# Performance work log

Measured on AMD Instinct MI355X. Metric: run time of the kernel, lower is better.

Reference implementation:

```python
import jax, jax.numpy as jnp
import numpy as np

DIM = 64
HEADS = 16
HEAD_DIM = DIM // HEADS  # 4
CHUNK = 128
LN_EPS = 1e-5


def _ln(v, w, b):
    mu = jnp.mean(v, axis=-1, keepdims=True)
    var = jnp.var(v, axis=-1, keepdims=True)
    return (v - mu) * jax.lax.rsqrt(var + LN_EPS) * w + b


def setup_inputs() -> dict:
    key = jax.random.key(0)
    ks = jax.random.split(key, 16)
    B, C, H, W = 8, 64, 128, 128
    s = 0.02
    inp = {
        "x": jax.random.normal(ks[0], (B, C, H, W), jnp.float32),
        "text_embed": jax.random.normal(ks[1], (B, C, H, W), jnp.float32),
        # Linear weights stored as [in, out] (torch uses [out, in]; math identical via x @ W)
        "q_w": jax.random.normal(ks[2], (DIM, DIM), jnp.float32) * s,
        "q_b": jnp.zeros((DIM,), jnp.float32),
        "k_w": jax.random.normal(ks[3], (DIM, DIM), jnp.float32) * s,
        "k_b": jnp.zeros((DIM,), jnp.float32),
        "v_w": jax.random.normal(ks[4], (DIM, DIM), jnp.float32) * s,
        "v_b": jnp.zeros((DIM,), jnp.float32),
        "o_w": jax.random.normal(ks[5], (DIM, DIM), jnp.float32) * s,
        "o_b": jnp.zeros((DIM,), jnp.float32),
        "ln1_w": jnp.ones((DIM,), jnp.float32),
        "ln1_b": jnp.zeros((DIM,), jnp.float32),
        "ln2_w": jnp.ones((DIM,), jnp.float32),
        "ln2_b": jnp.zeros((DIM,), jnp.float32),
        "fc1_w": jax.random.normal(ks[6], (DIM, 4 * DIM), jnp.float32) * s,
        "fc1_b": jnp.zeros((4 * DIM,), jnp.float32),
        "fc2_w": jax.random.normal(ks[7], (4 * DIM, DIM), jnp.float32) * s,
        "fc2_b": jnp.zeros((DIM,), jnp.float32),
        # 1x1 conv as [out_ch, in_ch]
        "conv_w": jax.random.normal(ks[8], (DIM, DIM), jnp.float32) * s,
        "conv_b": jnp.zeros((DIM,), jnp.float32),
        # FiLM MLP: pooled_channels=64*4*4=1024 -> 128 -> 128
        "m1_w": jax.random.normal(ks[9], (1024, 2 * DIM), jnp.float32) * s,
        "m1_b": jnp.zeros((2 * DIM,), jnp.float32),
        "m2_w": jax.random.normal(ks[10], (2 * DIM, 2 * DIM), jnp.float32) * s,
        "m2_b": jnp.zeros((2 * DIM,), jnp.float32),
    }
    return inp


def reference(x, text_embed, q_w, q_b, k_w, k_b, v_w, v_b, o_w, o_b,
              ln1_w, ln1_b, ln2_w, ln2_b, fc1_w, fc1_b, fc2_w, fc2_b,
              conv_w, conv_b, m1_w, m1_b, m2_w, m2_b):
    B, C, H, W = x.shape
    N = H * W
    Nc = N // CHUNK  # number of local chunks (block-diagonal attention)
    scale = jnp.sqrt(jnp.float32(HEAD_DIM))

    prior_flat = text_embed.reshape(B, C, N).transpose(0, 2, 1)  # [B,N,C]
    x_flat = x.reshape(B, C, N).transpose(0, 2, 1)               # [B,N,C]

    prior_norm = _ln(prior_flat, ln1_w, ln1_b)
    Q = prior_norm @ q_w + q_b
    K = x_flat @ k_w + k_b
    V = x_flat @ v_w + v_b

    # blocked heads: [B, Nc, CHUNK, HEADS, HEAD_DIM]
    Qb = Q.reshape(B, Nc, CHUNK, HEADS, HEAD_DIM)
    Kb = K.reshape(B, Nc, CHUNK, HEADS, HEAD_DIM)
    Vb = V.reshape(B, Nc, CHUNK, HEADS, HEAD_DIM)

    scores = jnp.einsum('bnqhd,bnkhd->bnhqk', Qb, Kb) / scale  # [B,Nc,H,CHUNK,CHUNK]
    probs = jax.nn.softmax(scores, axis=-1)
    attn = jnp.einsum('bnhqk,bnkhd->bnqhd', probs, Vb).reshape(B, N, DIM)

    attn = attn @ o_w + o_b
    h = attn + prior_flat
    h_norm = _ln(h, ln2_w, ln2_b)
    ffn = jax.nn.gelu(h_norm @ fc1_w + fc1_b, approximate=False) @ fc2_w + fc2_b
    h = ffn + h

    h4 = h.transpose(0, 2, 1).reshape(B, DIM, H, W)
    conv = jnp.einsum('bihw,oi->bohw', h4, conv_w) + conv_b[None, :, None, None]
    out = conv + x  # TIAM output

    # FiLM: adaptive_avg_pool2d to (4,4) (H,W divisible by 4)
    te = text_embed.reshape(B, C, 4, H // 4, 4, W // 4).mean(axis=(3, 5))  # [B,C,4,4]
    te = te.reshape(B, -1)  # [B, 1024]
    hmlp = jax.nn.leaky_relu(te @ m1_w + m1_b, negative_slope=0.01)
    gb = hmlp @ m2_w + m2_b  # [B, 128]
    gamma = gb[:, :DIM][:, :, None, None]
    beta = gb[:, DIM:][:, :, None, None]
    return (1.0 + gamma) * out + beta
```

## Files before the change

kernel.cpp:

```cpp
#include <hip/hip_runtime.h>
#include <hip/hip_bf16.h>

#define NB 8
#define NTOK 16384
#define TOTTOK (NB*NTOK)

typedef __hip_bfloat16 bf16;
typedef __attribute__((ext_vector_type(8))) short bfrag;
typedef __attribute__((ext_vector_type(4))) float ffrag;

#define MFMA(a,b,c) __builtin_amdgcn_mfma_f32_16x16x32_bf16(a,b,c,0,0,0)

__device__ __forceinline__ float b2f(bf16 v){ return __bfloat162float(v); }
__device__ __forceinline__ bf16 f2b(float v){ return __float2bfloat16(v); }
__device__ __forceinline__ float bfu(unsigned short u){
    union { float f; unsigned v; } x; x.v = ((unsigned)u) << 16; return x.f; }
__device__ __forceinline__ unsigned short ubits(float f){
    union { bf16 b; unsigned short u; } x; x.b = __float2bfloat16(f); return x.u; }
__device__ __forceinline__ unsigned short bu(bf16 b){
    union { bf16 b; unsigned short u; } x; x.b = b; return x.u; }
__device__ __forceinline__ void ld4(const bf16* p, float* f){
    uint2 r = *(const uint2*)p;
    f[0]=bfu(r.x & 0xffff); f[1]=bfu(r.x >> 16); f[2]=bfu(r.y & 0xffff); f[3]=bfu(r.y >> 16);
}
__device__ __forceinline__ bfrag ld_frag(const bf16* p, int stride){
    int lane = threadIdx.x & 63;
    return *(const bfrag*)(p + (lane & 15)*stride + (lane >> 4)*8);
}

#define WI_QKV   0
#define WI_OW    13824
#define WI_CW    18432
#define WI_W1    23040
#define WI_W2    41472
#define WI_CONST 57856
#define WI_TOT   58752

__global__ __launch_bounds__(256) void wprep_kernel(
    const float* __restrict__ qw, const float* __restrict__ kw, const float* __restrict__ vw,
    const float* __restrict__ ow, const float* __restrict__ cw,
    const float* __restrict__ w1, const float* __restrict__ w2,
    const float* __restrict__ ln1w, const float* __restrict__ ln1b,
    const float* __restrict__ qb, const float* __restrict__ kb_, const float* __restrict__ vb,
    const float* __restrict__ ob, const float* __restrict__ ln2w, const float* __restrict__ ln2b,
    const float* __restrict__ b1, const float* __restrict__ b2, const float* __restrict__ cb,
    bf16* __restrict__ WI)
{
    int gid = blockIdx.x*256 + threadIdx.x;
    if (gid >= WI_TOT) return;
    float v = 0.f;
    if (gid < WI_OW){
        int m = gid / 4608, r = gid % 4608;
        int o = r / 72, ii = r % 72;
        const float* src = (m==0)? qw : (m==1)? kw : vw;
        if (ii < 64) v = src[ii*64 + o];
    } else if (gid < WI_CW){
        int r = gid - WI_OW;
        int o = r / 72, ii = r % 72;
        if (ii < 64) v = ow[ii*64 + o];
    } else if (gid < WI_W1){
        int r = gid - WI_CW;
        int co = r / 72, ii = r % 72;
        if (ii < 64) v = cw[co*64 + ii];
    } else if (gid < WI_W2){
        int r = gid - WI_W1;
        int gg = r / 2304, rr = r % 2304;
        int ol = rr / 72, ii = rr % 72;
        if (ii < 64) v = w1[ii*256 + gg*32 + ol];
    } else if (gid < WI_CONST){
        int a = gid - WI_W2;
        int o = a >> 8, ra = a & 255;
        int blk = ra >> 3, wi = ra & 7;
        int k = ((blk ^ (o & 7)) << 3) | wi;
        v = w2[k*64 + o];
    } else {
        int r = gid - WI_CONST;
        if      (r <  64) v = ln1w[r];
        else if (r < 128) v = ln1b[r-64];
        else if (r < 192) v = qb[r-128];
        else if (r < 256) v = kb_[r-192];
        else if (r < 320) v = vb[r-256];
        else if (r < 384) v = ob[r-320];
        else if (r < 448) v = ln2w[r-384];
        else if (r < 512) v = ln2b[r-448];
        else if (r < 768) v = b1[r-512];
        else if (r < 832) v = b2[r-768];
        else              v = cb[r-832];
    }
    WI[gid] = f2b(v);
}

__global__ __launch_bounds__(256) void transpose_kernel(
    const float* __restrict__ x, const float* __restrict__ te,
    bf16* __restrict__ xT, bf16* __restrict__ teT, float* __restrict__ pool)
{
    __shared__ bf16 T[64*66];
    int blk = blockIdx.x;
    int tile = blk & 255, b = blk >> 8;
    int t0 = tile * 64;
    const size_t sbase = (size_t)b*64*NTOK + t0;
    const size_t obase = ((size_t)b*NTOK + t0)*64;
    int tid = threadIdx.x;
    #pragma unroll
    for (int p = 0; p < 4; ++p){
        int c = p*16 + (tid >> 4), j4 = (tid & 15)*4;
        float4 v = *(const float4*)(x + sbase + (size_t)c*NTOK + j4);
        bf16* tp = T + c*66 + j4;
        tp[0]=f2b(v.x); tp[1]=f2b(v.y); tp[2]=f2b(v.z); tp[3]=f2b(v.w);
    }
    __syncthreads();
    #pragma unroll
    for (int p = 0; p < 4; ++p){
        int j = p*16 + (tid >> 4), c4 = (tid & 15)*4;
        uint2 o;
        o.x = (unsigned)bu(T[(c4+0)*66 + j]) | ((unsigned)bu(T[(c4+1)*66 + j]) << 16);
        o.y = (unsigned)bu(T[(c4+2)*66 + j]) | ((unsigned)bu(T[(c4+3)*66 + j]) << 16);
        *(uint2*)(xT + obase + (size_t)j*64 + c4) = o;
    }
    __syncthreads();
    #pragma unroll
    for (int p = 0; p < 4; ++p){
        int c = p*16 + (tid >> 4), j4 = (tid & 15)*4;
        float4 v = *(const float4*)(te + sbase + (size_t)c*NTOK + j4);
        bf16* tp = T + c*66 + j4;
        tp[0]=f2b(v.x); tp[1]=f2b(v.y); tp[2]=f2b(v.z); tp[3]=f2b(v.w);
    }
    __syncthreads();
    #pragma unroll
    for (int p = 0; p < 4; ++p){
        int j = p*16 + (tid >> 4), c4 = (tid & 15)*4;
        uint2 o;
        o.x = (unsigned)bu(T[(c4+0)*66 + j]) | ((unsigned)bu(T[(c4+1)*66 + j]) << 16);
        o.y = (unsigned)bu(T[(c4+2)*66 + j]) | ((unsigned)bu(T[(c4+3)*66 + j]) << 16);
        *(uint2*)(teT + obase + (size_t)j*64 + c4) = o;
    }
    if (tid < 128){
        int c = tid >> 1, hf = tid & 1;
        float s = 0.f;
        #pragma unroll
        for (int u = 0; u < 32; ++u) s += b2f(T[c*66 + hf*32 + u]);
        int h = t0 >> 7;
        int w0 = t0 & 127;
        int region = (h >> 5)*4 + ((w0 + hf*32) >> 5);
        atomicAdd(pool + b*1024 + c*16 + region, s);
    }
}

__global__ __launch_bounds__(128) void film_kernel(const float* __restrict__ pool,
        const float* __restrict__ m1w, const float* __restrict__ m1b,
        const float* __restrict__ m2w, const float* __restrict__ m2b,
        float* __restrict__ gb){
    int b = blockIdx.x; int j = threadIdx.x;
    __shared__ float tel[1024];
    __shared__ float hm[128];
    for (int i = j; i < 1024; i += 128) tel[i] = pool[b*1024 + i] * (1.f/1024.f);
    __syncthreads();
    float s = m1b[j];
    for (int i = 0; i < 1024; ++i) s = fmaf(tel[i], m1w[i*128 + j], s);
    hm[j] = (s > 0.f) ? s : 0.01f*s;
    __syncthreads();
    float g = m2b[j];
    for (int i = 0; i < 128; ++i) g = fmaf(hm[i], m2w[i*128 + j], g);
    gb[b*128 + j] = g;
}

#define OFF_TE2 0
#define OFF_XT  16384
#define OFF_PN  34816
#define OFF_WT  53248
#define OFF_W2T 47616
#define OFF_CON 80896
#define SCALE_Q 0.72134752044448170f

__device__ __forceinline__ void ln_phase(const bf16* S, bf16* D,
                                         const bf16* Wt, const bf16* Bs, int tid)
{
    int tok = tid >> 1, hf = tid & 1;
    float vals[32];
    float s = 0.f, s2 = 0.f;
    #pragma unroll
    for (int u8 = 0; u8 < 4; ++u8){
        int k = (u8 + tok) & 3;
        uint4 v = *(const uint4*)(S + tok*64 + hf*32 + k*8);
        const unsigned* ap = &v.x;
        float* vp = vals + u8*8;
        #pragma unroll
        for (int e = 0; e < 4; ++e){
            float lo = bfu(ap[e] & 0xffff), hi = bfu(ap[e] >> 16);
            vp[e*2] = lo; vp[e*2+1] = hi;
            s += lo + hi;
            s2 = fmaf(lo, lo, fmaf(hi, hi, s2));
        }
    }
    s  += __shfl_xor(s, 1, 64);
    s2 += __shfl_xor(s2, 1, 64);
    float mean = s * (1.f/64.f);
    float var  = s2 * (1.f/64.f) - mean*mean;
    float rstd = rsqrtf(var + 1e-5f);
    #pragma unroll
    for (int u8 = 0; u8 < 4; ++u8){
        int k = (u8 + tok) & 3;
        int cc0 = hf*32 + k*8;
        uint4 wv = *(const uint4*)(Wt + cc0);
        uint4 bv = *(const uint4*)(Bs + cc0);
        const unsigned* wp = &wv.x;
        const unsigned* bp = &bv.x;
        uint4 o; unsigned* op = &o.x;
        #pragma unroll
        for (int e = 0; e < 4; ++e){
            float lo = (vals[u8*8+e*2]  -mean)*rstd*bfu(wp[e] & 0xffff) + bfu(bp[e] & 0xffff);
            float hi = (vals[u8*8+e*2+1]-mean)*rstd*bfu(wp[e] >> 16)    + bfu(bp[e] >> 16);
            op[e] = (unsigned)ubits(lo) | ((unsigned)ubits(hi) << 16);
        }
        *(uint4*)(D + tok*72 + cc0) = o;
    }
}

__global__ __launch_bounds__(256,2) void mega_kernel(
    const bf16* __restrict__ xT, const bf16* __restrict__ teT, const float* __restrict__ x,
    const bf16* __restrict__ WI, const float* __restrict__ gb, float* __restrict__ out)
{
    __shared__ __align__(16) char sm[81920];
    bf16* TE2 = (bf16*)(sm + OFF_TE2);
    bf16* XT  = (bf16*)(sm + OFF_XT);
    bf16* PN  = (bf16*)(sm + OFF_PN);
    bf16* WT  = (bf16*)(sm + OFF_WT);
    bf16* VT  = (bf16*)(sm + OFF_WT);
    bf16* OWT = (bf16*)(sm + OFF_WT);
    bf16* W1S = (bf16*)(sm + OFF_PN);
    bf16* P   = (bf16*)(sm + OFF_PN + 4608);
    bf16* CWs = (bf16*)(sm + OFF_PN);
    bf16* W2T = (bf16*)(sm + OFF_W2T);
    bf16* CON = (bf16*)(sm + OFF_CON);
    bf16* OT  = (bf16*)(sm + OFF_TE2);

    int tid = threadIdx.x;
    int w = tid >> 6, lane = tid & 63;
    int g = lane >> 4, c = lane & 15;
    int t0g = blockIdx.x * 128;
    int b = t0g >> 14, n0 = t0g & (NTOK-1);
    const ffrag fz = {0.f,0.f,0.f,0.f};

    {
        const uint4* gx = (const uint4*)(xT + (size_t)t0g*64);
        const uint4* gt = (const uint4*)(teT + (size_t)t0g*64);
        #pragma unroll
        for (int p = 0; p < 4; ++p){
            int i = tid + p*256;
            int tok = i >> 3, seg = i & 7;
            *(uint4*)(XT + tok*72 + seg*8) = gx[i];
            ((uint4*)TE2)[i] = gt[i];
        }
        const uint4* wq = (const uint4*)(WI + WI_QKV);
        for (int i = tid; i < 1728; i += 256) ((uint4*)WT)[i] = wq[i];
        if (tid < 16) ((uint4*)CON)[tid] = ((const uint4*)(WI + WI_CONST))[tid];
    }
    __syncthreads();
    ln_phase(TE2, PN, CON, CON + 64, tid);
    __syncthreads();
    {
        if (tid < 24) ((uint4*)CON)[tid] = ((const uint4*)(WI + WI_CONST + 128))[tid];
        ffrag accQ[2][4], accK[2][4], accV[2][4];
        #pragma unroll
        for (int mi=0;mi<2;++mi) for (int nt=0;nt<4;++nt){ accQ[mi][nt]=fz; accK[mi][nt]=fz; accV[mi][nt]=fz; }
        bfrag aQ[2][2], aX[2][2];
        #pragma unroll
        for (int mi=0;mi<2;++mi) for (int k2=0;k2<2;++k2){
            aQ[mi][k2] = ld_frag(PN + (w*32 + mi*16)*72 + k2*32, 72);
            aX[mi][k2] = ld_frag(XT + (w*32 + mi*16)*72 + k2*32, 72);
        }
        for (int nt = 0; nt < 4; ++nt){
            #pragma unroll
            for (int k2 = 0; k2 < 2; ++k2){
                bfrag bq2 = ld_frag(WT +        nt*16*72 + k2*32, 72);
                bfrag bk2 = ld_frag(WT + 4608 + nt*16*72 + k2*32, 72);
                bfrag bv2 = ld_frag(WT + 9216 + nt*16*72 + k2*32, 72);
                #pragma unroll
                for (int mi=0;mi<2;++mi){
                    accQ[mi][nt] = MFMA(aQ[mi][k2], bq2, accQ[mi][nt]);
                    accK[mi][nt] = MFMA(aX[mi][k2], bk2, accK[mi][nt]);
                    accV[mi][nt] = MFMA(aX[mi][k2], bv2, accV[mi][nt]);
                }
            }
        }
        __syncthreads();
        int rq = g*4;
        #pragma unroll
        for (int mi=0;mi<2;++mi) for (int nt=0;nt<4;++nt){
            int n = nt*16 + c;
            float bq3 = b2f(CON[n]), bk3 = b2f(CON[64+n]), bv3 = b2f(CON[128+n]);
            #pragma unroll
            for (int r=0;r<4;++r){
                int m = w*32 + mi*16 + rq + r;
                PN[m*72 + n] = f2b((accQ[mi][nt][r] + bq3) * SCALE_Q);
                XT[m*72 + n] = f2b(accK[mi][nt][r] + bk3);
                int kp = (m & 15)*8 + (m >> 4);
                VT[(5*(n>>2) + (n&3))*136 + kp] = f2b(accV[mi][nt][r] + bv3);
            }
        }
        {
            int row = 5*(tid >> 4) + 4, col8 = (tid & 15)*8;
            uint4 ov; ov.x = ov.y = ov.z = ov.w = 0x3f803f80u;
            *(uint4*)(VT + row*136 + col8) = ov;
        }
    }
    __syncthreads();
    {
        int kb = w >> 1;
        bfrag bq[8];
        #pragma unroll
        for (int nt = 0; nt < 8; ++nt) bq[nt] = ld_frag(XT + nt*16*72 + kb*32, 72);
        __syncthreads();
        bf16* Pw = XT + w*2048;
        #pragma unroll 1
        for (int hh = 0; hh < 4; ++hh){
            int h = w*4 + hh;
            int ag = (h & 7) >> 1;
            bfrag bv4[4];
            #pragma unroll
            for (int ks = 0; ks < 4; ++ks) bv4[ks] = ld_frag(VT + (5*h)*136 + ks*32, 136);
            #pragma unroll 2
            for (int qt = 0; qt < 8; ++qt){
                int q = qt*16 + c;
                uint2 qv = *(const uint2*)(PN + q*72 + h*4);
                union { bfrag f; uint2 u[2]; } A;
                uint2 z2; z2.x = 0u; z2.y = 0u;
                uint2 sel = (g == ag) ? qv : z2;
                if (hh & 1){ A.u[0] = z2;  A.u[1] = sel; }
                else       { A.u[0] = sel; A.u[1] = z2;  }
                ffrag acc[8];
                #pragma unroll
                for (int nt = 0; nt < 8; ++nt) acc[nt] = MFMA(A.f, bq[nt], fz);
                #pragma unroll
                for (int nt = 0; nt < 8; ++nt){
                    #pragma unroll
                    for (int r = 0; r < 4; ++r) acc[nt][r] = exp2f(acc[nt][r]);
                }
                #pragma unroll
                for (int r = 0; r < 4; ++r){
                    uint4 pk;
                    pk.x = (unsigned)ubits(acc[0][r]) | ((unsigned)ubits(acc[1][r]) << 16);
                    pk.y = (unsigned)ubits(acc[2][r]) | ((unsigned)ubits(acc[3][r]) << 16);
                    pk.z = (unsigned)ubits(acc[4][r]) | ((unsigned)ubits(acc[5][r]) << 16);
                    pk.w = (unsigned)ubits(acc[6][r]) | ((unsigned)ubits(acc[7][r]) << 16);
                    int row = 4*g + r;
                    *(uint4*)(Pw + row*128 + (((c ^ row) & 15) << 3)) = pk;
                }
                ffrag og = fz;
                #pragma unroll
                for (int ks = 0; ks < 4; ++ks){
                    bfrag ap = *(const bfrag*)(Pw + c*128 + ((((ks*4 + g) ^ c) & 15) << 3));
                    og = MFMA(ap, bv4[ks], og);
                }
                #pragma unroll
                for (int r = 0; r < 4; ++r){
                    float lr = __shfl(og[r], (lane & 48) | 4, 64);
                    if (c < 4)
                        PN[(qt*16 + 4*g + r)*72 + h*4 + c] = f2b(og[r] / lr);
                }
            }
        }
    }
    __syncthreads();
    {
        const uint4* oi = (const uint4*)(WI + WI_OW);
        for (int i = tid; i < 576; i += 256) ((uint4*)OWT)[i] = oi[i];
        if (tid < 24) ((uint4*)CON)[tid] = ((const uint4*)(WI + WI_CONST + 320))[tid];
        __syncthreads();
        ffrag acc2[2][4];
        #pragma unroll
        for (int mi=0;mi<2;++mi) for (int nt=0;nt<4;++nt) acc2[mi][nt] = fz;
        bfrag af2[2][2];
        #pragma unroll
        for (int mi=0;mi<2;++mi) for (int k2=0;k2<2;++k2)
            af2[mi][k2] = ld_frag(PN + (w*32 + mi*16)*72 + k2*32, 72);
        #pragma unroll
        for (int nt=0;nt<4;++nt){
            #pragma unroll
            for (int k2=0;k2<2;++k2){
                bfrag bf_ = ld_frag(OWT + nt*16*72 + k2*32, 72);
                #pragma unroll
                for (int mi=0;mi<2;++mi) acc2[mi][nt] = MFMA(af2[mi][k2], bf_, acc2[mi][nt]);
            }
        }
        __syncthreads();
        int rq = g*4;
        #pragma unroll
        for (int mi=0;mi<2;++mi) for (int nt=0;nt<4;++nt){
            int n = nt*16 + c;
            float bo = b2f(CON[n]);
            #pragma unroll
            for (int r=0;r<4;++r){
                int m = w*32 + mi*16 + rq + r;
                XT[m*72 + n] = f2b(acc2[mi][nt][r] + bo);
            }
        }
    }
    __syncthreads();
    for (int j = tid; j < 1024; j += 256){
        int tok = j >> 3, c8 = (j & 7)*8;
        uint4 a = *(const uint4*)(TE2 + tok*64 + c8);
        uint4 bq = *(const uint4*)(XT + tok*72 + c8);
        const unsigned* ap = &a.x; const unsigned* bp = &bq.x;
        uint4 o; unsigned* op = &o.x;
        #pragma unroll
        for (int e = 0; e < 4; ++e){
            float lo = bfu(ap[e] & 0xffff) + bfu(bp[e] & 0xffff);
            float hi = bfu(ap[e] >> 16)    + bfu(bp[e] >> 16);
            op[e] = (unsigned)ubits(lo) | ((unsigned)ubits(hi) << 16);
        }
        *(uint4*)(TE2 + tok*64 + c8) = o;
    }
    __syncthreads();
    ln_phase(TE2, XT, CON + 64, CON + 128, tid);
    __syncthreads();
    {
        const uint4* w2i = (const uint4*)(WI + WI_W2);
        for (int i = tid; i < 2048; i += 256) ((uint4*)W2T)[i] = w2i[i];
        if (tid < 48) ((uint4*)CON)[tid] = ((const uint4*)(WI + WI_CONST + 512))[tid];
        bfrag af[2][2];
        #pragma unroll
        for (int mi=0;mi<2;++mi) for (int k2=0;k2<2;++k2)
            af[mi][k2] = ld_frag(XT + (w*32 + mi*16)*72 + k2*32, 72);
        ffrag acc2[2][4];
        #pragma unroll
        for (int mi=0;mi<2;++mi) for (int nt=0;nt<4;++nt) acc2[mi][nt] = fz;
        int rq = g*4;
        const uint4* w1i = (const uint4*)(WI + WI_W1);
        uint4 pA = w1i[tid];
        uint4 pB = pA;
        if (tid < 32) pB = w1i[256 + tid];
        for (int gg = 0; gg < 8; ++gg){
            __syncthreads();
            ((uint4*)W1S)[tid] = pA;
            if (tid < 32) ((uint4*)W1S)[256 + tid] = pB;
            if (gg < 7){
                pA = w1i[(gg+1)*288 + tid];
                if (tid < 32) pB = w1i[(gg+1)*288 + 256 + tid];
            }
            __syncthreads();
            ffrag accg[2][2];
            #pragma unroll
            for (int mi=0;mi<2;++mi) for (int ntl=0;ntl<2;++ntl) accg[mi][ntl] = fz;
            #pragma unroll
            for (int ntl=0;ntl<2;++ntl){
                #pragma unroll
                for (int k2=0;k2<2;++k2){
                    bfrag bf_ = ld_frag(W1S + ntl*16*72 + k2*32, 72);
                    #pragma unroll
                    for (int mi=0;mi<2;++mi) accg[mi][ntl] = MFMA(af[mi][k2], bf_, accg[mi][ntl]);
                }
            }
            #pragma unroll
            for (int mi=0;mi<2;++mi) for (int ntl=0;ntl<2;++ntl){
                int n = ntl*16 + c;
                float bb = b2f(CON[gg*32 + n]);
                #pragma unroll
                for (int r=0;r<4;++r){
                    int m = w*32 + mi*16 + rq + r;
                    float xv = accg[mi][ntl][r] + bb;
                    P[m*32 + ((((n>>3) ^ ((m>>1)&3)) << 3) | (n & 7))] =
                        f2b(0.5f*xv*(1.f + erff(xv*0.70710678118654752f)));
                }
            }
            #pragma unroll
            for (int mi=0;mi<2;++mi){
                int rr = w*32 + mi*16 + c;
                bfrag ap = *(const bfrag*)(P + rr*32 + ((g ^ ((rr>>1)&3)) << 3));
                #pragma unroll
                for (int nt=0;nt<4;++nt){
                    int n = nt*16 + c;
                    int chunk = gg*4 + g;
                    bfrag bf2 = *(const bfrag*)(W2T + n*256 + ((chunk ^ (n&7)) << 3));
                    acc2[mi][nt] = MFMA(ap, bf2, acc2[mi][nt]);
                }
            }
        }
        #pragma unroll
        for (int mi=0;mi<2;++mi) for (int nt=0;nt<4;++nt){
            int n = nt*16 + c;
            float bb = b2f(CON[256+n]);
            #pragma unroll
            for (int r=0;r<4;++r){
                int m = w*32 + mi*16 + rq + r;
                XT[m*72 + n] = f2b(acc2[mi][nt][r] + bb + b2f(TE2[m*64 + n]));
            }
        }
    }
    __syncthreads();
    {
        const uint4* ci = (const uint4*)(WI + WI_CW);
        for (int i = tid; i < 576; i += 256) ((uint4*)CWs)[i] = ci[i];
        __syncthreads();
        bfrag ac[2];
        #pragma unroll
        for (int k2=0;k2<2;++k2) ac[k2] = ld_frag(CWs + (w*16)*72 + k2*32, 72);
        int rq = g*4;
        for (int nt = 0; nt < 8; ++nt){
            ffrag accc = fz;
            #pragma unroll
            for (int k2=0;k2<2;++k2){
                bfrag bh = ld_frag(XT + nt*16*72 + k2*32, 72);
                accc = MFMA(ac[k2], bh, accc);
            }
            int tok = nt*16 + c;
            #pragma unroll
            for (int r=0;r<4;++r){
                int co = w*16 + rq + r;
                OT[co*128 + tok] = f2b(accc[r] + b2f(CON[320+co]));
            }
        }
    }
    __syncthreads();
    {
        int cc = tid >> 2, seg = (tid & 3)*32;
        float gamma = 1.f + gb[b*128 + cc];
        float beta  = gb[b*128 + 64 + cc];
        const size_t gbase = (size_t)b*64*NTOK + (size_t)cc*NTOK + n0 + seg;
        #pragma unroll
        for (int u = 0; u < 8; ++u){
            float cv[4];
            ld4(OT + cc*128 + seg + u*4, cv);
            float4 xv = *(const float4*)(x + gbase + u*4);
            float4 ov;
            ov.x = fmaf(gamma, cv[0]+xv.x, beta);
            ov.y = fmaf(gamma, cv[1]+xv.y, beta);
            ov.z = fmaf(gamma, cv[2]+xv.z, beta);
            ov.w = fmaf(gamma, cv[3]+xv.w, beta);
            *(float4*)(out + gbase + u*4) = ov;
        }
    }
}

extern "C" void kernel_launch(void* const* d_in, const int* in_sizes, int n_in,
                              void* d_out, int out_size, void* d_ws, size_t ws_size,
                              hipStream_t stream){
    const float* x   = (const float*)d_in[0];
    const float* te  = (const float*)d_in[1];
    const float* qw  = (const float*)d_in[2];
    const float* qb  = (const float*)d_in[3];
    const float* kw  = (const float*)d_in[4];
    const float* kb  = (const float*)d_in[5];
    const float* vw  = (const float*)d_in[6];
    const float* vb  = (const float*)d_in[7];
    const float* ow  = (const float*)d_in[8];
    const float* ob  = (const float*)d_in[9];
    const float* ln1w= (const float*)d_in[10];
    const float* ln1b= (const float*)d_in[11];
    const float* ln2w= (const float*)d_in[12];
    const float* ln2b= (const float*)d_in[13];
    const float* w1  = (const float*)d_in[14];
    const float* b1  = (const float*)d_in[15];
    const float* w2  = (const float*)d_in[16];
    const float* b2  = (const float*)d_in[17];
    const float* cw  = (const float*)d_in[18];
    const float* cb  = (const float*)d_in[19];
    const float* m1w = (const float*)d_in[20];
    const float* m1b = (const float*)d_in[21];
    const float* m2w = (const float*)d_in[22];
    const float* m2b = (const float*)d_in[23];

    char* ws = (char*)d_ws;
    const size_t BUF = (size_t)TOTTOK*64*2;
    bf16* xT  = (bf16*)(ws);
    bf16* teT = (bf16*)(ws + BUF);
    float* pool = (float*)(ws + 2*BUF);
    float* gbp  = (float*)(ws + 2*BUF + 32768);
    bf16* WI    = (bf16*)(ws + 2*BUF + 36864);

    hipMemsetAsync(pool, 0, 8*1024*sizeof(float), stream);
    wprep_kernel<<<(WI_TOT + 255)/256, 256, 0, stream>>>(
        qw, kw, vw, ow, cw, w1, w2,
        ln1w, ln1b, qb, kb, vb, ob, ln2w, ln2b, b1, b2, cb, WI);
    transpose_kernel<<<2048, 256, 0, stream>>>(x, te, xT, teT, pool);
    film_kernel<<<8, 128, 0, stream>>>(pool, m1w, m1b, m2w, m2b, gbp);
    mega_kernel<<<TOTTOK/128, 256, 0, stream>>>(xT, teT, x, WI, gbp, (float*)d_out);
}
```

Measured before the change: 350.5 us.

## Double fused-kernel block to 512 threads and use fast GELU approximation

The fused per-chunk kernel now runs with 512 threads (8 waves) per 128-token block instead of 256. Each wave owns 16 rows instead of 32, and the attention, LN, conv and output phases are re-partitioned to match, including new V and P layouts. The exact erf GELU is replaced by a sigmoid-style exp2/rcp approximation, and the division in the softmax normalisation becomes a hardware reciprocal. This aims to raise wave-level parallelism and cut transcendental cost, at the price of more synchronisation per block, small accuracy loss, and register pressure from the tighter launch bounds.

After: 317.2 us. 1.11x faster.

```diff
diff --git a/kernel.cpp b/kernel.cpp
--- a/kernel.cpp
+++ b/kernel.cpp
@@ -22,6 +22,15 @@
 __device__ __forceinline__ void ld4(const bf16* p, float* f){
     uint2 r = *(const uint2*)p;
     f[0]=bfu(r.x & 0xffff); f[1]=bfu(r.x >> 16); f[2]=bfu(r.y & 0xffff); f[3]=bfu(r.y >> 16);
+}
+__device__ __forceinline__ float fastrcp(float x){
+    float r; asm("v_rcp_f32 %0, %1" : "=v"(r) : "v"(x)); return r; }
+__device__ __forceinline__ float gelu_t(float x){
+    float x2 = x*x;
+    float y  = x * fmaf(x2, 0.1029425f, 2.3022077f);
+    float z  = exp2f(y);
+    float rc = fastrcp(z + 1.f);
+    return x - x*rc;
 }
 __device__ __forceinline__ bfrag ld_frag(const bf16* p, int stride){
     int lane = threadIdx.x & 63;
@@ -175,13 +184,15 @@
 __device__ __forceinline__ void ln_phase(const bf16* S, bf16* D,
                                          const bf16* Wt, const bf16* Bs, int tid)
 {
-    int tok = tid >> 1, hf = tid & 1;
-    float vals[32];
+    int tok = tid >> 2, q4 = tid & 3;
+    float vals[16];
+    int op2[2];
     float s = 0.f, s2 = 0.f;
     #pragma unroll
-    for (int u8 = 0; u8 < 4; ++u8){
-        int k = (u8 + tok) & 3;
-        uint4 v = *(const uint4*)(S + tok*64 + hf*32 + k*8);
+    for (int u8 = 0; u8 < 2; ++u8){
+        int o = (q4*2 + u8) ^ (tok & 7);
+        op2[u8] = o;
+        uint4 v = *(const uint4*)(S + tok*64 + o*8);
         const unsigned* ap = &v.x;
         float* vp = vals + u8*8;
         #pragma unroll
@@ -192,31 +203,30 @@
             s2 = fmaf(lo, lo, fmaf(hi, hi, s2));
         }
     }
-    s  += __shfl_xor(s, 1, 64);
-    s2 += __shfl_xor(s2, 1, 64);
+    s  += __shfl_xor(s, 1, 64);  s2 += __shfl_xor(s2, 1, 64);
+    s  += __shfl_xor(s, 2, 64);  s2 += __shfl_xor(s2, 2, 64);
     float mean = s * (1.f/64.f);
     float var  = s2 * (1.f/64.f) - mean*mean;
     float rstd = rsqrtf(var + 1e-5f);
     #pragma unroll
-    for (int u8 = 0; u8 < 4; ++u8){
-        int k = (u8 + tok) & 3;
-        int cc0 = hf*32 + k*8;
+    for (int u8 = 0; u8 < 2; ++u8){
+        int cc0 = op2[u8]*8;
         uint4 wv = *(const uint4*)(Wt + cc0);
         uint4 bv = *(const uint4*)(Bs + cc0);
         const unsigned* wp = &wv.x;
         const unsigned* bp = &bv.x;
-        uint4 o; unsigned* op = &o.x;
+        uint4 o; unsigned* opp = &o.x;
         #pragma unroll
         for (int e = 0; e < 4; ++e){
             float lo = (vals[u8*8+e*2]  -mean)*rstd*bfu(wp[e] & 0xffff) + bfu(bp[e] & 0xffff);
             float hi = (vals[u8*8+e*2+1]-mean)*rstd*bfu(wp[e] >> 16)    + bfu(bp[e] >> 16);
-            op[e] = (unsigned)ubits(lo) | ((unsigned)ubits(hi) << 16);
+            opp[e] = (unsigned)ubits(lo) | ((unsigned)ubits(hi) << 16);
         }
         *(uint4*)(D + tok*72 + cc0) = o;
     }
 }
 
-__global__ __launch_bounds__(256,2) void mega_kernel(
+__global__ __launch_bounds__(512,4) void mega_kernel(
     const bf16* __restrict__ xT, const bf16* __restrict__ teT, const float* __restrict__ x,
     const bf16* __restrict__ WI, const float* __restrict__ gb, float* __restrict__ out)
 {
@@ -245,14 +255,14 @@
         const uint4* gx = (const uint4*)(xT + (size_t)t0g*64);
         const uint4* gt = (const uint4*)(teT + (size_t)t0g*64);
         #pragma unroll
-        for (int p = 0; p < 4; ++p){
-            int i = tid + p*256;
+        for (int p = 0; p < 2; ++p){
+            int i = tid + p*512;
             int tok = i >> 3, seg = i & 7;
             *(uint4*)(XT + tok*72 + seg*8) = gx[i];
             ((uint4*)TE2)[i] = gt[i];
         }
         const uint4* wq = (const uint4*)(WI + WI_QKV);
-        for (int i = tid; i < 1728; i += 256) ((uint4*)WT)[i] = wq[i];
+        for (int i = tid; i < 1728; i += 512) ((uint4*)WT)[i] = wq[i];
         if (tid < 16) ((uint4*)CON)[tid] = ((const uint4*)(WI + WI_CONST))[tid];
     }
     __syncthreads();
@@ -260,14 +270,14 @@
     __syncthreads();
     {
         if (tid < 24) ((uint4*)CON)[tid] = ((const uint4*)(WI + WI_CONST + 128))[tid];
-        ffrag accQ[2][4], accK[2][4], accV[2][4];
-        #pragma unroll
-        for (int mi=0;mi<2;++mi) for (int nt=0;nt<4;++nt){ accQ[mi][nt]=fz; accK[mi][nt]=fz; accV[mi][nt]=fz; }
-        bfrag aQ[2][2], aX[2][2];
-        #pragma unroll
-        for (int mi=0;mi<2;++mi) for (int k2=0;k2<2;++k2){
-            aQ[mi][k2] = ld_frag(PN + (w*32 + mi*16)*72 + k2*32, 72);
-            aX[mi][k2] = ld_frag(XT + (w*32 + mi*16)*72 + k2*32, 72);
+        ffrag accQ[4], accK[4], accV[4];
+        #pragma unroll
+        for (int nt=0;nt<4;++nt){ accQ[nt]=fz; accK[nt]=fz; accV[nt]=fz; }
+        bfrag aQ[2], aX[2];
+        #pragma unroll
+        for (int k2=0;k2<2;++k2){
+            aQ[k2] = ld_frag(PN + (w*16)*72 + k2*32, 72);
+            aX[k2] = ld_frag(XT + (w*16)*72 + k2*32, 72);
         }
         for (int nt = 0; nt < 4; ++nt){
             #pragma unroll
@@ -275,30 +285,27 @@
                 bfrag bq2 = ld_frag(WT +        nt*16*72 + k2*32, 72);
                 bfrag bk2 = ld_frag(WT + 4608 + nt*16*72 + k2*32, 72);
                 bfrag bv2 = ld_frag(WT + 9216 + nt*16*72 + k2*32, 72);
-                #pragma unroll
-                for (int mi=0;mi<2;++mi){
-                    accQ[mi][nt] = MFMA(aQ[mi][k2], bq2, accQ[mi][nt]);
-                    accK[mi][nt] = MFMA(aX[mi][k2], bk2, accK[mi][nt]);
-                    accV[mi][nt] = MFMA(aX[mi][k2], bv2, accV[mi][nt]);
-                }
+                accQ[nt] = MFMA(aQ[k2], bq2, accQ[nt]);
+                accK[nt] = MFMA(aX[k2], bk2, accK[nt]);
+                accV[nt] = MFMA(aX[k2], bv2, accV[nt]);
             }
         }
         __syncthreads();
         int rq = g*4;
         #pragma unroll
-        for (int mi=0;mi<2;++mi) for (int nt=0;nt<4;++nt){
+        for (int nt=0;nt<4;++nt){
             int n = nt*16 + c;
             float bq3 = b2f(CON[n]), bk3 = b2f(CON[64+n]), bv3 = b2f(CON[128+n]);
             #pragma unroll
             for (int r=0;r<4;++r){
-                int m = w*32 + mi*16 + rq + r;
-                PN[m*72 + n] = f2b((accQ[mi][nt][r] + bq3) * SCALE_Q);
-                XT[m*72 + n] = f2b(accK[mi][nt][r] + bk3);
-                int kp = (m & 15)*8 + (m >> 4);
-                VT[(5*(n>>2) + (n&3))*136 + kp] = f2b(accV[mi][nt][r] + bv3);
-            }
-        }
-        {
+                int m = w*16 + rq + r;
+                PN[m*72 + n] = f2b((accQ[nt][r] + bq3) * SCALE_Q);
+                XT[m*72 + n] = f2b(accK[nt][r] + bk3);
+                int kp = ((m >> 6) << 6) + (m & 15)*4 + ((m >> 4) & 3);
+                VT[(5*(n>>2) + (n&3))*136 + kp] = f2b(accV[nt][r] + bv3);
+            }
+        }
+        if (tid < 256){
             int row = 5*(tid >> 4) + 4, col8 = (tid & 15)*8;
             uint4 ov; ov.x = ov.y = ov.z = ov.w = 0x3f803f80u;
             *(uint4*)(VT + row*136 + col8) = ov;
@@ -306,19 +313,19 @@
     }
     __syncthreads();
     {
-        int kb = w >> 1;
         bfrag bq[8];
         #pragma unroll
-        for (int nt = 0; nt < 8; ++nt) bq[nt] = ld_frag(XT + nt*16*72 + kb*32, 72);
+        for (int nt = 0; nt < 8; ++nt) bq[nt] = ld_frag(XT + nt*16*72 + (w>>2)*32, 72);
         __syncthreads();
-        bf16* Pw = XT + w*2048;
+        bf16* Pw = XT + w*1024;
         #pragma unroll 1
-        for (int hh = 0; hh < 4; ++hh){
-            int h = w*4 + hh;
-            int ag = (h & 7) >> 1;
+        for (int hh = 0; hh < 2; ++hh){
+            int h = w*2 + hh;
+            int ag = w & 3;
             bfrag bv4[4];
             #pragma unroll
-            for (int ks = 0; ks < 4; ++ks) bv4[ks] = ld_frag(VT + (5*h)*136 + ks*32, 136);
+            for (int kk = 0; kk < 4; ++kk)
+                bv4[kk] = ld_frag(VT + (5*h)*136 + (kk>>1)*64 + (kk&1)*32, 136);
             #pragma unroll 2
             for (int qt = 0; qt < 8; ++qt){
                 int q = qt*16 + c;
@@ -326,37 +333,38 @@
                 union { bfrag f; uint2 u[2]; } A;
                 uint2 z2; z2.x = 0u; z2.y = 0u;
                 uint2 sel = (g == ag) ? qv : z2;
-                if (hh & 1){ A.u[0] = z2;  A.u[1] = sel; }
-                else       { A.u[0] = sel; A.u[1] = z2;  }
-                ffrag acc[8];
-                #pragma unroll
-                for (int nt = 0; nt < 8; ++nt) acc[nt] = MFMA(A.f, bq[nt], fz);
-                #pragma unroll
-                for (int nt = 0; nt < 8; ++nt){
-                    #pragma unroll
-                    for (int r = 0; r < 4; ++r) acc[nt][r] = exp2f(acc[nt][r]);
-                }
-                #pragma unroll
-                for (int r = 0; r < 4; ++r){
-                    uint4 pk;
-                    pk.x = (unsigned)ubits(acc[0][r]) | ((unsigned)ubits(acc[1][r]) << 16);
-                    pk.y = (unsigned)ubits(acc[2][r]) | ((unsigned)ubits(acc[3][r]) << 16);
-                    pk.z = (unsigned)ubits(acc[4][r]) | ((unsigned)ubits(acc[5][r]) << 16);
-                    pk.w = (unsigned)ubits(acc[6][r]) | ((unsigned)ubits(acc[7][r]) << 16);
-                    int row = 4*g + r;
-                    *(uint4*)(Pw + row*128 + (((c ^ row) & 15) << 3)) = pk;
-                }
+                if (hh){ A.u[0] = z2;  A.u[1] = sel; }
+                else   { A.u[0] = sel; A.u[1] = z2;  }
                 ffrag og = fz;
                 #pragma unroll
-                for (int ks = 0; ks < 4; ++ks){
-                    bfrag ap = *(const bfrag*)(Pw + c*128 + ((((ks*4 + g) ^ c) & 15) << 3));
-                    og = MFMA(ap, bv4[ks], og);
+                for (int kh = 0; kh < 2; ++kh){
+                    ffrag acc[4];
+                    #pragma unroll
+                    for (int nt = 0; nt < 4; ++nt) acc[nt] = MFMA(A.f, bq[kh*4+nt], fz);
+                    #pragma unroll
+                    for (int nt = 0; nt < 4; ++nt){
+                        #pragma unroll
+                        for (int r = 0; r < 4; ++r) acc[nt][r] = exp2f(acc[nt][r]);
+                    }
+                    #pragma unroll
+                    for (int r = 0; r < 4; ++r){
+                        uint2 pk;
+                        pk.x = (unsigned)ubits(acc[0][r]) | ((unsigned)ubits(acc[1][r]) << 16);
+                        pk.y = (unsigned)ubits(acc[2][r]) | ((unsigned)ubits(acc[3][r]) << 16);
+                        int row = 4*g + r;
+                        *(uint2*)(Pw + row*64 + (((c>>1) ^ (row&7)) << 3) + ((c&1) << 2)) = pk;
+                    }
+                    #pragma unroll
+                    for (int ks = 0; ks < 2; ++ks){
+                        bfrag ap = *(const bfrag*)(Pw + c*64 + (((ks*4 + g) ^ (c&7)) << 3));
+                        og = MFMA(ap, bv4[kh*2 + ks], og);
+                    }
                 }
                 #pragma unroll
                 for (int r = 0; r < 4; ++r){
                     float lr = __shfl(og[r], (lane & 48) | 4, 64);
                     if (c < 4)
-                        PN[(qt*16 + 4*g + r)*72 + h*4 + c] = f2b(og[r] / lr);
+                        PN[(qt*16 + 4*g + r)*72 + h*4 + c] = f2b(og[r] * fastrcp(lr));
                 }
             }
         }
@@ -364,50 +372,49 @@
     __syncthreads();
     {
         const uint4* oi = (const uint4*)(WI + WI_OW);
-        for (int i = tid; i < 576; i += 256) ((uint4*)OWT)[i] = oi[i];
+        for (int i = tid; i < 576; i += 512) ((uint4*)OWT)[i] = oi[i];
         if (tid < 24) ((uint4*)CON)[tid] = ((const uint4*)(WI + WI_CONST + 320))[tid];
         __syncthreads();
-        ffrag acc2[2][4];
-        #pragma unroll
-        for (int mi=0;mi<2;++mi) for (int nt=0;nt<4;++nt) acc2[mi][nt] = fz;
-        bfrag af2[2][2];
-        #pragma unroll
-        for (int mi=0;mi<2;++mi) for (int k2=0;k2<2;++k2)
-            af2[mi][k2] = ld_frag(PN + (w*32 + mi*16)*72 + k2*32, 72);
+        ffrag acc2[4];
+        #pragma unroll
+        for (int nt=0;nt<4;++nt) acc2[nt] = fz;
+        bfrag af2[2];
+        #pragma unroll
+        for (int k2=0;k2<2;++k2)
+            af2[k2] = ld_frag(PN + (w*16)*72 + k2*32, 72);
         #pragma unroll
         for (int nt=0;nt<4;++nt){
             #pragma unroll
             for (int k2=0;k2<2;++k2){
                 bfrag bf_ = ld_frag(OWT + nt*16*72 + k2*32, 72);
-                #pragma unroll
-                for (int mi=0;mi<2;++mi) acc2[mi][nt] = MFMA(af2[mi][k2], bf_, acc2[mi][nt]);
+                acc2[nt] = MFMA(af2[k2], bf_, acc2[nt]);
             }
         }
         __syncthreads();
         int rq = g*4;
         #pragma unroll
-        for (int mi=0;mi<2;++mi) for (int nt=0;nt<4;++nt){
+        for (int nt=0;nt<4;++nt){
             int n = nt*16 + c;
             float bo = b2f(CON[n]);
             #pragma unroll
             for (int r=0;r<4;++r){
-                int m = w*32 + mi*16 + rq + r;
-                XT[m*72 + n] = f2b(acc2[mi][nt][r] + bo);
-            }
-        }
-    }
-    __syncthreads();
-    for (int j = tid; j < 1024; j += 256){
+                int m = w*16 + rq + r;
+                XT[m*72 + n] = f2b(acc2[nt][r] + bo);
+            }
+        }
+    }
+    __syncthreads();
+    for (int j = tid; j < 1024; j += 512){
         int tok = j >> 3, c8 = (j & 7)*8;
         uint4 a = *(const uint4*)(TE2 + tok*64 + c8);
-        uint4 bq = *(const uint4*)(XT + tok*72 + c8);
-        const unsigned* ap = &a.x; const unsigned* bp = &bq.x;
-        uint4 o; unsigned* op = &o.x;
+        uint4 bq2 = *(const uint4*)(XT + tok*72 + c8);
+        const unsigned* ap = &a.x; const unsigned* bp = &bq2.x;
+        uint4 o; unsigned* opp = &o.x;
         #pragma unroll
         for (int e = 0; e < 4; ++e){
             float lo = bfu(ap[e] & 0xffff) + bfu(bp[e] & 0xffff);
             float hi = bfu(ap[e] >> 16)    + bfu(bp[e] >> 16);
-            op[e] = (unsigned)ubits(lo) | ((unsigned)ubits(hi) << 16);
+            opp[e] = (unsigned)ubits(lo) | ((unsigned)ubits(hi) << 16);
         }
         *(uint4*)(TE2 + tok*64 + c8) = o;
     }
@@ -416,87 +423,83 @@
     __syncthreads();
     {
         const uint4* w2i = (const uint4*)(WI + WI_W2);
-        for (int i = tid; i < 2048; i += 256) ((uint4*)W2T)[i] = w2i[i];
+        for (int i = tid; i < 2048; i += 512) ((uint4*)W2T)[i] = w2i[i];
         if (tid < 48) ((uint4*)CON)[tid] = ((const uint4*)(WI + WI_CONST + 512))[tid];
-        bfrag af[2][2];
-        #pragma unroll
-        for (int mi=0;mi<2;++mi) for (int k2=0;k2<2;++k2)
-            af[mi][k2] = ld_frag(XT + (w*32 + mi*16)*72 + k2*32, 72);
-        ffrag acc2[2][4];
-        #pragma unroll
-        for (int mi=0;mi<2;++mi) for (int nt=0;nt<4;++nt) acc2[mi][nt] = fz;
+        bfrag af[2];
+        #pragma unroll
+        for (int k2=0;k2<2;++k2)
+            af[k2] = ld_frag(XT + (w*16)*72 + k2*32, 72);
+        ffrag acc2[4];
+        #pragma unroll
+        for (int nt=0;nt<4;++nt) acc2[nt] = fz;
         int rq = g*4;
         const uint4* w1i = (const uint4*)(WI + WI_W1);
-        uint4 pA = w1i[tid];
-        uint4 pB = pA;
-        if (tid < 32) pB = w1i[256 + tid];
+        uint4 pA;
+        if (tid < 288) pA = w1i[tid];
         for (int gg = 0; gg < 8; ++gg){
             __syncthreads();
-            ((uint4*)W1S)[tid] = pA;
-            if (tid < 32) ((uint4*)W1S)[256 + tid] = pB;
-            if (gg < 7){
-                pA = w1i[(gg+1)*288 + tid];
-                if (tid < 32) pB = w1i[(gg+1)*288 + 256 + tid];
+            if (tid < 288){
+                ((uint4*)W1S)[tid] = pA;
+                if (gg < 7) pA = w1i[(gg+1)*288 + tid];
             }
             __syncthreads();
-            ffrag accg[2][2];
-            #pragma unroll
-            for (int mi=0;mi<2;++mi) for (int ntl=0;ntl<2;++ntl) accg[mi][ntl] = fz;
+            ffrag accg[2];
+            #pragma unroll
+            for (int ntl=0;ntl<2;++ntl) accg[ntl] = fz;
             #pragma unroll
             for (int ntl=0;ntl<2;++ntl){
                 #pragma unroll
                 for (int k2=0;k2<2;++k2){
                     bfrag bf_ = ld_frag(W1S + ntl*16*72 + k2*32, 72);
-                    #pragma unroll
-                    for (int mi=0;mi<2;++mi) accg[mi][ntl] = MFMA(af[mi][k2], bf_, accg[mi][ntl]);
+                    accg[ntl] = MFMA(af[k2], bf_, accg[ntl]);
                 }
             }
             #pragma unroll
-            for (int mi=0;mi<2;++mi) for (int ntl=0;ntl<2;++ntl){
+            for (int ntl=0;ntl<2;++ntl){
                 int n = ntl*16 + c;
                 float bb = b2f(CON[gg*32 + n]);
                 #pragma unroll
                 for (int r=0;r<4;++r){
-                    int m = w*32 + mi*16 + rq + r;
-                    float xv = accg[mi][ntl][r] + bb;
-                    P[m*32 + ((((n>>3) ^ ((m>>1)&3)) << 3) | (n & 7))] =
-                        f2b(0.5f*xv*(1.f + erff(xv*0.70710678118654752f)));
+                    int m = w*16 + rq + r;
+                    float xv = accg[ntl][r] + bb;
+                    P[m*32 + ((((n>>3) ^ ((m>>1)&3)) << 3) | (n & 7))] = f2b(gelu_t(xv));
                 }
             }
-            #pragma unroll
-            for (int mi=0;mi<2;++mi){
-                int rr = w*32 + mi*16 + c;
+            {
+                int rr = w*16 + c;
                 bfrag ap = *(const bfrag*)(P + rr*32 + ((g ^ ((rr>>1)&3)) << 3));
                 #pragma unroll
                 for (int nt=0;nt<4;++nt){
                     int n = nt*16 + c;
                     int chunk = gg*4 + g;
                     bfrag bf2 = *(const bfrag*)(W2T + n*256 + ((chunk ^ (n&7)) << 3));
-                    acc2[mi][nt] = MFMA(ap, bf2, acc2[mi][nt]);
+                    acc2[nt] = MFMA(ap, bf2, acc2[nt]);
                 }
             }
         }
         #pragma unroll
-        for (int mi=0;mi<2;++mi) for (int nt=0;nt<4;++nt){
+        for (int nt=0;nt<4;++nt){
             int n = nt*16 + c;
             float bb = b2f(CON[256+n]);
             #pragma unroll
             for (int r=0;r<4;++r){
-                int m = w*32 + mi*16 + rq + r;
-                XT[m*72 + n] = f2b(acc2[mi][nt][r] + bb + b2f(TE2[m*64 + n]));
+                int m = w*16 + rq + r;
+                XT[m*72 + n] = f2b(acc2[nt][r] + bb + b2f(TE2[m*64 + n]));
             }
         }
     }
     __syncthreads();
     {
         const uint4* ci = (const uint4*)(WI + WI_CW);
-        for (int i = tid; i < 576; i += 256) ((uint4*)CWs)[i] = ci[i];
+        for (int i = tid; i < 576; i += 512) ((uint4*)CWs)[i] = ci[i];
         __syncthreads();
         bfrag ac[2];
         #pragma unroll
-        for (int k2=0;k2<2;++k2) ac[k2] = ld_frag(CWs + (w*16)*72 + k2*32, 72);
+        for (int k2=0;k2<2;++k2) ac[k2] = ld_frag(CWs + ((w&3)*16)*72 + k2*32, 72);
         int rq = g*4;
-        for (int nt = 0; nt < 8; ++nt){
+        #pragma unroll
+        for (int nt4 = 0; nt4 < 4; ++nt4){
+            int nt = (w>>2)*4 + nt4;
             ffrag accc = fz;
             #pragma unroll
             for (int k2=0;k2<2;++k2){
@@ -506,19 +509,19 @@
             int tok = nt*16 + c;
             #pragma unroll
             for (int r=0;r<4;++r){
-                int co = w*16 + rq + r;
+                int co = (w&3)*16 + rq + r;
                 OT[co*128 + tok] = f2b(accc[r] + b2f(CON[320+co]));
             }
         }
     }
     __syncthreads();
     {
-        int cc = tid >> 2, seg = (tid & 3)*32;
+        int cc = tid >> 3, seg = (tid & 7)*16;
         float gamma = 1.f + gb[b*128 + cc];
         float beta  = gb[b*128 + 64 + cc];
         const size_t gbase = (size_t)b*64*NTOK + (size_t)cc*NTOK + n0 + seg;
         #pragma unroll
-        for (int u = 0; u < 8; ++u){
+        for (int u = 0; u < 4; ++u){
             float cv[4];
             ld4(OT + cc*128 + seg + u*4, cv);
             float4 xv = *(const float4*)(x + gbase + u*4);
@@ -574,5 +577,5 @@
         ln1w, ln1b, qb, kb, vb, ob, ln2w, ln2b, b1, b2, cb, WI);
     transpose_kernel<<<2048, 256, 0, stream>>>(x, te, xT, teT, pool);
     film_kernel<<<8, 128, 0, stream>>>(pool, m1w, m1b, m2w, m2b, gbp);
-    mega_kernel<<<TOTTOK/128, 256, 0, stream>>>(xT, teT, x, WI, gbp, (float*)d_out);
-}
+    mega_kernel<<<TOTTOK/128, 512, 0, stream>>>(xT, teT, x, WI, gbp, (float*)d_out);
+}
```
